# Optimization experiments

Measured on AMD Instinct MI355X. Metric: run time of the kernel, lower is better.

Reference implementation:

```python
import jax, jax.numpy as jnp
import numpy as np

K = 3       # kernel_size
STRIDE = 1
PAD = 1
EPS = 1e-12  # F.normalize eps


def setup_inputs() -> dict:
    key = jax.random.key(0)
    k1, k2, k3 = jax.random.split(key, 3)
    x = jax.random.normal(k1, (8, 128, 112, 112), dtype=jnp.float32)
    weight = jax.random.normal(k2, (256, 128, K, K), dtype=jnp.float32)
    bias = jax.random.normal(k3, (256,), dtype=jnp.float32)
    return {"x": x, "weight": weight, "bias": bias}


def reference(x, weight, bias):
    B, C, H, W = x.shape
    Cout = weight.shape[0]
    oh = (H + 2 * PAD - K) // STRIDE + 1
    ow = (W + 2 * PAD - K) // STRIDE + 1
    # im2col: [B, C*K*K, oh, ow]; feature order (C, kh, kw), same as torch F.unfold
    patches = jax.lax.conv_general_dilated_patches(
        x, (K, K), (STRIDE, STRIDE), [(PAD, PAD), (PAD, PAD)],
        dimension_numbers=("NCHW", "OIHW", "NCHW"))
    u = patches.reshape(B, C * K * K, oh * ow)
    # L2-normalize each patch column (dim=1), matching F.normalize(p=2, dim=1)
    norm = jnp.sqrt(jnp.sum(u * u, axis=1, keepdims=True))
    u = u / jnp.maximum(norm, EPS)
    # GEMM: [Cout, C*K*K] x [B, C*K*K, L] -> [B, Cout, L]
    out = jnp.einsum("od,bdl->bol", weight.reshape(Cout, -1), u)
    out = out.reshape(B, Cout, oh, ow) + bias[None, :, None, None]
    return out
```

## Files before the change

### kernel.cpp

```cpp
#include <hip/hip_runtime.h>

#define CIN    128
#define COUT   256
#define Hh     112
#define Ww     112
#define HW     12544
#define NBATCH 8
#define NPIX   (NBATCH*HW)
#define KD     (CIN*9)
#define PH     114
#define PPIX   (NBATCH*PH*PH)

typedef __bf16         v8bf __attribute__((ext_vector_type(8)));
typedef float          v4f  __attribute__((ext_vector_type(4)));

__device__ __forceinline__ unsigned short f2bf(float f) {
  unsigned int u = __float_as_uint(f);
  u += 0x7FFFu + ((u >> 16) & 1u);
  return (unsigned short)(u >> 16);
}

__device__ __forceinline__ void gl_lds16(const void* g, void* l) {
  __builtin_amdgcn_global_load_lds(
      (const __attribute__((address_space(1))) void*)g,
      (__attribute__((address_space(3))) void*)l, 16, 0, 0);
}

#define USS 130
__global__ __launch_bounds__(256) void k_pre(
    const float* __restrict__ x, const float* __restrict__ w,
    unsigned short* __restrict__ xbp, unsigned short* __restrict__ wpk,
    float* __restrict__ sq)
{
  __shared__ unsigned short US[112 * USS];
  __shared__ float sqp[112 * 4];

  int tid = threadIdx.x;
  int bid = blockIdx.x;

  if (bid >= NBATCH * PH) {
    int t = (bid - NBATCH * PH) * 2048 + tid * 8;
#pragma unroll
    for (int i = 0; i < 8; ++i) {
      int idx = t + i;
      int o  = idx / KD;
      int rr = idx - o * KD;
      int kk = rr >> 7;
      int c  = rr & 127;
      wpk[idx] = f2bf(w[(size_t)o * KD + c * 9 + kk]);
    }
    return;
  }

  int b  = bid / PH;
  int py = bid - b * PH;
  unsigned int* dstrow = (unsigned int*)xbp +
      (size_t)(b * PH + py) * PH * (CIN / 2);

  if (py == 0 || py == PH - 1) {
    uint4 z = {0, 0, 0, 0};
    for (int h = tid; h < PH * (CIN / 8); h += 256)
      *(uint4*)(dstrow + h * 4) = z;
    return;
  }

  int oy  = py - 1;
  int l   = tid & 63;
  int wid = tid >> 6;
  const float* xp = x + (size_t)b * CIN * HW + (size_t)oy * Ww;
  bool valid = l < 56;

  float a0 = 0.0f, a1 = 0.0f;
#pragma unroll
  for (int it = 0; it < 32; ++it) {
    int c = wid * 32 + it;
    float vx = 0.0f, vy = 0.0f;
    if (valid) {
      float2 v = *(const float2*)(xp + (size_t)c * HW + 2 * l);
      vx = v.x; vy = v.y;
    }
    a0 += vx * vx;
    a1 += vy * vy;
    if (valid) {
      US[(2 * l) * USS + c]     = f2bf(vx);
      US[(2 * l + 1) * USS + c] = f2bf(vy);
    }
  }
  if (valid) { sqp[(2 * l) * 4 + wid] = a0; sqp[(2 * l + 1) * 4 + wid] = a1; }
  __syncthreads();

  if (tid < 112) {
    float s = sqp[tid * 4] + sqp[tid * 4 + 1] + sqp[tid * 4 + 2] + sqp[tid * 4 + 3];
    sq[(size_t)b * HW + (size_t)oy * Ww + tid] = s;
  }

  unsigned int* dst = dstrow + (CIN / 2);
  for (int h = tid; h < 112 * 16; h += 256) {
    int px = h >> 4, part = h & 15;
    const unsigned short* s = &US[px * USS + part * 8];
    uint4 vv;
    vv.x = *(const unsigned int*)(s + 0);
    vv.y = *(const unsigned int*)(s + 2);
    vv.z = *(const unsigned int*)(s + 4);
    vv.w = *(const unsigned int*)(s + 6);
    *(uint4*)(dst + h * 4) = vv;
  }

  if (tid < 32) {
    uint4 z = {0, 0, 0, 0};
    int px   = (tid >> 4) ? (PH - 1) : 0;
    int part = tid & 15;
    *(uint4*)(dstrow + px * (CIN / 2) + part * 4) = z;
  }
}

#define SLAB_S 132
__global__ __launch_bounds__(256, 3) void k_conv(
    const unsigned short* __restrict__ wp,
    const unsigned short* __restrict__ xbp,
    const float* __restrict__ sq,
    const float* __restrict__ bias,
    float* __restrict__ out)
{
  __shared__ __align__(16) char smem[64 * SLAB_S * 4];
  unsigned short* As = (unsigned short*)smem;
  unsigned short* Bs = As + 128 * 64;
  float* slab = (float*)smem;

  int tid  = threadIdx.x;
  int lane = tid & 63;
  int wid  = tid >> 6;
  int wm   = wid >> 1, wn = wid & 1;
  int quad = lane >> 4;
  int l16  = lane & 15;

  int L  = blockIdx.x;
  int g  = L >> 4;
  int j  = L & 15;
  int bn = g * 8 + (j & 7);
  int bm = j >> 3;

  int srow = tid >> 3;
  int g16  = (tid & 7) ^ (srow & 7);

  const unsigned short* asrc = wp + (size_t)(bm * 128 + srow) * KD + g16 * 8;

  int pb[4];
#pragma unroll
  for (int jj = 0; jj < 4; ++jj) {
    int n  = bn * 128 + jj * 32 + srow;
    int b  = n / HW;  int r  = n - b * HW;
    int oy = r / Ww;  int ox = r - oy * Ww;
    pb[jj] = ((b * PH + oy) * PH + ox) * CIN + g16 * 8;
  }

  v4f acc[4][4];
#pragma unroll
  for (int mt = 0; mt < 4; ++mt)
#pragma unroll
    for (int nt = 0; nt < 4; ++nt)
#pragma unroll
      for (int q = 0; q < 4; ++q) acc[mt][nt][q] = 0.0f;

  const int khs[9] = {0,0,0,1,1,1,2,2,2};
  const int kws[9] = {0,1,2,0,1,2,0,1,2};

  for (int s = 0; s < 18; ++s) {
    int kk   = s >> 1;
    int c0   = (s & 1) * 64;
    int soff = (khs[kk] * PH + kws[kk]) * CIN + c0;

#pragma unroll
    for (int jj = 0; jj < 4; ++jj)
      gl_lds16(asrc + (size_t)jj * 32 * KD + s * 64,
               &As[(wid * 8 + jj * 32) * 64]);
#pragma unroll
    for (int jj = 0; jj < 4; ++jj)
      gl_lds16(xbp + pb[jj] + soff,
               &Bs[(wid * 8 + jj * 32) * 64]);

    __syncthreads();

#pragma unroll
    for (int h = 0; h < 2; ++h) {
      v8bf af[4], bf[4];
      int cch = (h * 4 + quad) ^ (l16 & 7);
#pragma unroll
      for (int mt = 0; mt < 4; ++mt)
        af[mt] = *(const v8bf*)&As[(wm * 64 + mt * 16 + l16) * 64 + cch * 8];
#pragma unroll
      for (int nt = 0; nt < 4; ++nt)
        bf[nt] = *(const v8bf*)&Bs[(wn * 64 + nt * 16 + l16) * 64 + cch * 8];
#pragma unroll
      for (int mt = 0; mt < 4; ++mt)
#pragma unroll
        for (int nt = 0; nt < 4; ++nt)
          acc[mt][nt] = __builtin_amdgcn_mfma_f32_16x16x32_bf16(
              af[mt], bf[nt], acc[mt][nt], 0, 0, 0);
    }

    __syncthreads();
  }

  int nbase = bn * 128;

  float invv[4];
#pragma unroll
  for (int nt = 0; nt < 4; ++nt) {
    int n  = nbase + wn * 64 + nt * 16 + l16;
    int b  = n / HW;  int r  = n - b * HW;
    int oy = r / Ww;  int ox = r - oy * Ww;
    const float* s = sq + (size_t)b * HW;
    float a2 = 0.0f;
#pragma unroll
    for (int dy = -1; dy <= 1; ++dy) {
      int iy = oy + dy;
      if (iy < 0 || iy >= Hh) continue;
#pragma unroll
      for (int dx = -1; dx <= 1; ++dx) {
        int ix = ox + dx;
        if (ix < 0 || ix >= Ww) continue;
        a2 += s[iy * Ww + ix];
      }
    }
    invv[nt] = 1.0f / fmaxf(sqrtf(a2), 1e-12f);
  }

  int bb = nbase / HW;
  int rr = nbase - bb * HW;
  float* obase = out + (size_t)bb * COUT * HW + rr;

  for (int pass = 0; pass < 2; ++pass) {
    if (pass) __syncthreads();
    if (wm == pass) {
#pragma unroll
      for (int mt = 0; mt < 4; ++mt)
#pragma unroll
        for (int nt = 0; nt < 4; ++nt) {
          int col = wn * 64 + nt * 16 + l16;
#pragma unroll
          for (int reg = 0; reg < 4; ++reg)
            slab[(mt * 16 + quad * 4 + reg) * SLAB_S + col] =
                acc[mt][nt][reg] * invv[nt];
        }
    }
    __syncthreads();
#pragma unroll
    for (int it = 0; it < 2; ++it) {
      int row = it * 32 + (tid >> 3);
      int o   = bm * 128 + pass * 64 + row;
      float bv = bias[o];
      float* orow = obase + (size_t)o * HW;
#pragma unroll
      for (int k = 0; k < 4; ++k) {
        int c4 = ((tid & 7) + k * 8) * 4;
        v4f v = *(const v4f*)&slab[row * SLAB_S + c4];
        v4f r2;
#pragma unroll
        for (int q = 0; q < 4; ++q) r2[q] = v[q] + bv;
        *(v4f*)(orow + c4) = r2;
      }
    }
  }
}

extern "C" void kernel_launch(void* const* d_in, const int* in_sizes, int n_in,
                              void* d_out, int out_size, void* d_ws, size_t ws_size,
                              hipStream_t stream) {
  const float* x    = (const float*)d_in[0];
  const float* w    = (const float*)d_in[1];
  const float* bias = (const float*)d_in[2];
  float* out        = (float*)d_out;

  char* ws = (char*)d_ws;
  unsigned short* xbp = (unsigned short*)ws;
  size_t off = (size_t)PPIX * CIN * 2;
  unsigned short* wpk = (unsigned short*)(ws + off);
  off += (size_t)COUT * KD * 2;
  float* sq = (float*)(ws + off);

  k_pre<<<NBATCH * PH + (COUT * KD) / 2048, 256, 0, stream>>>(x, w, xbp, wpk, sq);
  k_conv<<<1568, 256, 0, stream>>>(wpk, xbp, sq, bias, out);
}
```

Baseline: 217.2 us.

## Enlarge conv tile to 256x256 with double-buffered async LDS pipeline

The conv kernel moves from 128x128 tiles with 256 threads to 256x256 tiles with 512 threads, covering all output channels in one block (392 blocks). The K loop becomes double-buffered: it issues global-to-LDS loads for stage t+2 while computing stage t, using explicit vmcnt waits and raw barriers instead of full syncthreads, and raises MFMA priority with setprio. This is meant to hide load latency and double operand reuse per LDS byte, at the cost of 128KB of dynamic LDS, fewer blocks (under 1.3 waves on 256 CUs), and higher register pressure from 32 accumulators per thread.

```diff
diff --git a/kernel.cpp b/kernel.cpp
--- a/kernel.cpp
+++ b/kernel.cpp
@@ -114,95 +114,134 @@
   }
 }
 
-#define SLAB_S 132
-__global__ __launch_bounds__(256, 3) void k_conv(
+__device__ __forceinline__ void conv_tile(
+    unsigned short* Ab, unsigned short* Bb,
+    int t, bool do_stage,
+    v4f (&acc)[8][4], const int (&pb)[4],
+    const unsigned short* __restrict__ asrc,
+    const unsigned short* __restrict__ xbp,
+    int wm, int wn, int quad, int l16, int wid)
+{
+#pragma unroll
+  for (int h = 0; h < 2; ++h) {
+    v8bf bfr[4];
+    int cch = (h * 4 + quad) ^ (l16 & 7);
+#pragma unroll
+    for (int nt = 0; nt < 4; ++nt)
+      bfr[nt] = *(const v8bf*)&Bb[(wn * 64 + nt * 16 + l16) * 64 + cch * 8];
+#pragma unroll
+    for (int mh = 0; mh < 2; ++mh) {
+      v8bf af[4];
+#pragma unroll
+      for (int m2 = 0; m2 < 4; ++m2)
+        af[m2] = *(const v8bf*)&Ab[(wm * 128 + (mh * 4 + m2) * 16 + l16) * 64 + cch * 8];
+      __builtin_amdgcn_s_setprio(1);
+#pragma unroll
+      for (int m2 = 0; m2 < 4; ++m2)
+#pragma unroll
+        for (int nt = 0; nt < 4; ++nt)
+          acc[mh * 4 + m2][nt] = __builtin_amdgcn_mfma_f32_16x16x32_bf16(
+              af[m2], bfr[nt], acc[mh * 4 + m2][nt], 0, 0, 0);
+      __builtin_amdgcn_s_setprio(0);
+    }
+  }
+  __builtin_amdgcn_sched_barrier(0);
+  __builtin_amdgcn_s_barrier();
+  __builtin_amdgcn_sched_barrier(0);
+  if (do_stage) {
+    int t2 = t + 2;
+    int kk = t2 >> 1;
+    int kh = kk / 3, kw = kk - 3 * kh;
+    int soff = (kh * PH + kw) * CIN + (t2 & 1) * 64;
+#pragma unroll
+    for (int jj = 0; jj < 4; ++jj)
+      gl_lds16(asrc + (size_t)jj * 64 * KD + t2 * 64,
+               &Ab[(jj * 64 + wid * 8) * 64]);
+#pragma unroll
+    for (int jj = 0; jj < 4; ++jj)
+      gl_lds16(xbp + pb[jj] + soff,
+               &Bb[(jj * 64 + wid * 8) * 64]);
+    asm volatile("s_waitcnt vmcnt(8)" ::: "memory");
+  } else {
+    asm volatile("s_waitcnt vmcnt(0)" ::: "memory");
+  }
+  __builtin_amdgcn_sched_barrier(0);
+  __builtin_amdgcn_s_barrier();
+  __builtin_amdgcn_sched_barrier(0);
+}
+
+#define SLAB2 260
+__global__ __launch_bounds__(512, 2) void k_conv(
     const unsigned short* __restrict__ wp,
     const unsigned short* __restrict__ xbp,
     const float* __restrict__ sq,
     const float* __restrict__ bias,
     float* __restrict__ out)
 {
-  __shared__ __align__(16) char smem[64 * SLAB_S * 4];
-  unsigned short* As = (unsigned short*)smem;
-  unsigned short* Bs = As + 128 * 64;
+  extern __shared__ __align__(16) char smem[];
+  unsigned short* As0 = (unsigned short*)smem;
+  unsigned short* Bs0 = As0 + 256 * 64;
+  unsigned short* As1 = Bs0 + 256 * 64;
+  unsigned short* Bs1 = As1 + 256 * 64;
   float* slab = (float*)smem;
 
   int tid  = threadIdx.x;
   int lane = tid & 63;
   int wid  = tid >> 6;
-  int wm   = wid >> 1, wn = wid & 1;
+  int wm   = wid >> 2;
+  int wn   = wid & 3;
   int quad = lane >> 4;
   int l16  = lane & 15;
 
   int L  = blockIdx.x;
-  int g  = L >> 4;
-  int j  = L & 15;
-  int bn = g * 8 + (j & 7);
-  int bm = j >> 3;
+  int bn = (L & 7) * 49 + (L >> 3);
+  int nbase = bn * 256;
 
   int srow = tid >> 3;
   int g16  = (tid & 7) ^ (srow & 7);
 
-  const unsigned short* asrc = wp + (size_t)(bm * 128 + srow) * KD + g16 * 8;
+  const unsigned short* asrc = wp + (size_t)srow * KD + g16 * 8;
 
   int pb[4];
 #pragma unroll
   for (int jj = 0; jj < 4; ++jj) {
-    int n  = bn * 128 + jj * 32 + srow;
+    int n  = nbase + jj * 64 + srow;
     int b  = n / HW;  int r  = n - b * HW;
     int oy = r / Ww;  int ox = r - oy * Ww;
     pb[jj] = ((b * PH + oy) * PH + ox) * CIN + g16 * 8;
   }
 
-  v4f acc[4][4];
-#pragma unroll
-  for (int mt = 0; mt < 4; ++mt)
+  v4f acc[8][4];
+#pragma unroll
+  for (int mt = 0; mt < 8; ++mt)
 #pragma unroll
     for (int nt = 0; nt < 4; ++nt)
 #pragma unroll
       for (int q = 0; q < 4; ++q) acc[mt][nt][q] = 0.0f;
 
-  const int khs[9] = {0,0,0,1,1,1,2,2,2};
-  const int kws[9] = {0,1,2,0,1,2,0,1,2};
-
-  for (int s = 0; s < 18; ++s) {
-    int kk   = s >> 1;
-    int c0   = (s & 1) * 64;
-    int soff = (khs[kk] * PH + kws[kk]) * CIN + c0;
-
-#pragma unroll
-    for (int jj = 0; jj < 4; ++jj)
-      gl_lds16(asrc + (size_t)jj * 32 * KD + s * 64,
-               &As[(wid * 8 + jj * 32) * 64]);
-#pragma unroll
-    for (int jj = 0; jj < 4; ++jj)
-      gl_lds16(xbp + pb[jj] + soff,
-               &Bs[(wid * 8 + jj * 32) * 64]);
-
-    __syncthreads();
-
-#pragma unroll
-    for (int h = 0; h < 2; ++h) {
-      v8bf af[4], bf[4];
-      int cch = (h * 4 + quad) ^ (l16 & 7);
-#pragma unroll
-      for (int mt = 0; mt < 4; ++mt)
-        af[mt] = *(const v8bf*)&As[(wm * 64 + mt * 16 + l16) * 64 + cch * 8];
-#pragma unroll
-      for (int nt = 0; nt < 4; ++nt)
-        bf[nt] = *(const v8bf*)&Bs[(wn * 64 + nt * 16 + l16) * 64 + cch * 8];
-#pragma unroll
-      for (int mt = 0; mt < 4; ++mt)
-#pragma unroll
-        for (int nt = 0; nt < 4; ++nt)
-          acc[mt][nt] = __builtin_amdgcn_mfma_f32_16x16x32_bf16(
-              af[mt], bf[nt], acc[mt][nt], 0, 0, 0);
-    }
-
-    __syncthreads();
-  }
-
-  int nbase = bn * 128;
+#pragma unroll
+  for (int jj = 0; jj < 4; ++jj)
+    gl_lds16(asrc + (size_t)jj * 64 * KD, &As0[(jj * 64 + wid * 8) * 64]);
+#pragma unroll
+  for (int jj = 0; jj < 4; ++jj)
+    gl_lds16(xbp + pb[jj], &Bs0[(jj * 64 + wid * 8) * 64]);
+#pragma unroll
+  for (int jj = 0; jj < 4; ++jj)
+    gl_lds16(asrc + (size_t)jj * 64 * KD + 64, &As1[(jj * 64 + wid * 8) * 64]);
+#pragma unroll
+  for (int jj = 0; jj < 4; ++jj)
+    gl_lds16(xbp + pb[jj] + 64, &Bs1[(jj * 64 + wid * 8) * 64]);
+  asm volatile("s_waitcnt vmcnt(8)" ::: "memory");
+  __builtin_amdgcn_sched_barrier(0);
+  __builtin_amdgcn_s_barrier();
+  __builtin_amdgcn_sched_barrier(0);
+
+  for (int i = 0; i < 8; ++i) {
+    conv_tile(As0, Bs0, 2 * i,     true, acc, pb, asrc, xbp, wm, wn, quad, l16, wid);
+    conv_tile(As1, Bs1, 2 * i + 1, true, acc, pb, asrc, xbp, wm, wn, quad, l16, wid);
+  }
+  conv_tile(As0, Bs0, 16, false, acc, pb, asrc, xbp, wm, wn, quad, l16, wid);
+  conv_tile(As1, Bs1, 17, false, acc, pb, asrc, xbp, wm, wn, quad, l16, wid);
 
   float invv[4];
 #pragma unroll
@@ -230,36 +269,35 @@
   int rr = nbase - bb * HW;
   float* obase = out + (size_t)bb * COUT * HW + rr;
 
-  for (int pass = 0; pass < 2; ++pass) {
-    if (pass) __syncthreads();
-    if (wm == pass) {
-#pragma unroll
-      for (int mt = 0; mt < 4; ++mt)
+#pragma unroll
+  for (int p = 0; p < 4; ++p) {
+    if (p) __syncthreads();
+    if (wm == (p >> 1)) {
+      int base_mt = (p & 1) * 4;
+#pragma unroll
+      for (int m2 = 0; m2 < 4; ++m2)
 #pragma unroll
         for (int nt = 0; nt < 4; ++nt) {
           int col = wn * 64 + nt * 16 + l16;
 #pragma unroll
           for (int reg = 0; reg < 4; ++reg)
-            slab[(mt * 16 + quad * 4 + reg) * SLAB_S + col] =
-                acc[mt][nt][reg] * invv[nt];
+            slab[(m2 * 16 + quad * 4 + reg) * SLAB2 + col] =
+                acc[base_mt + m2][nt][reg] * invv[nt];
         }
     }
     __syncthreads();
-#pragma unroll
-    for (int it = 0; it < 2; ++it) {
-      int row = it * 32 + (tid >> 3);
-      int o   = bm * 128 + pass * 64 + row;
-      float bv = bias[o];
-      float* orow = obase + (size_t)o * HW;
-#pragma unroll
-      for (int k = 0; k < 4; ++k) {
-        int c4 = ((tid & 7) + k * 8) * 4;
-        v4f v = *(const v4f*)&slab[row * SLAB_S + c4];
-        v4f r2;
-#pragma unroll
-        for (int q = 0; q < 4; ++q) r2[q] = v[q] + bv;
-        *(v4f*)(orow + c4) = r2;
-      }
+    int r  = tid >> 3;
+    int o  = p * 64 + r;
+    float bv = bias[o];
+    float* orow = obase + (size_t)o * HW;
+#pragma unroll
+    for (int k = 0; k < 8; ++k) {
+      int c4 = (tid & 7) * 4 + k * 32;
+      v4f v = *(const v4f*)&slab[r * SLAB2 + c4];
+      v4f r2;
+#pragma unroll
+      for (int q = 0; q < 4; ++q) r2[q] = v[q] + bv;
+      *(v4f*)(orow + c4) = r2;
     }
   }
 }
@@ -279,6 +317,13 @@
   off += (size_t)COUT * KD * 2;
   float* sq = (float*)(ws + off);
 
+  static bool attr_done = false;
+  if (!attr_done) {
+    hipFuncSetAttribute((const void*)k_conv,
+                        hipFuncAttributeMaxDynamicSharedMemorySize, 131072);
+    attr_done = true;
+  }
+
   k_pre<<<NBATCH * PH + (COUT * KD) / 2048, 256, 0, stream>>>(x, w, xbp, wpk, sq);
-  k_conv<<<1568, 256, 0, stream>>>(wpk, xbp, sq, bias, out);
-}
+  k_conv<<<392, 512, 131072, stream>>>(wpk, xbp, sq, bias, out);
+}
```

After: 219.2 us. No clear change (+0.9%).

## Stage a shared input-row window in LDS and reuse it across kernel-width taps

Applied to the files above, without the earlier changes.

The conv kernel used to fetch a fresh 128-pixel by 64-channel B tile from global memory for each of the 18 (tap, channel-half) steps. It now loads one swizzled window of 144 padded pixel slots by all 128 channels per kernel row. Each per-lane B fragment is read at a per-pixel slot offset plus the kw shift, so the window serves all three horizontal taps. This cuts global and L2 traffic for activations roughly threefold. In exchange, LDS use grows to about 52 KB per block, which is tight for three blocks per CU, and the swizzled window reads may cause extra bank conflicts.

```diff
diff --git a/kernel.cpp b/kernel.cpp
--- a/kernel.cpp
+++ b/kernel.cpp
@@ -10,6 +10,7 @@
 #define KD     (CIN*9)
 #define PH     114
 #define PPIX   (NBATCH*PH*PH)
+#define WSLOT  144
 
 typedef __bf16         v8bf __attribute__((ext_vector_type(8)));
 typedef float          v4f  __attribute__((ext_vector_type(4)));
@@ -122,9 +123,9 @@
     const float* __restrict__ bias,
     float* __restrict__ out)
 {
-  __shared__ __align__(16) char smem[64 * SLAB_S * 4];
-  unsigned short* As = (unsigned short*)smem;
-  unsigned short* Bs = As + 128 * 64;
+  __shared__ __align__(16) char smem[WSLOT * CIN * 2 + 128 * 64 * 2];
+  unsigned short* win = (unsigned short*)smem;
+  unsigned short* As  = win + WSLOT * CIN;
   float* slab = (float*)smem;
 
   int tid  = threadIdx.x;
@@ -142,16 +143,21 @@
 
   int srow = tid >> 3;
   int g16  = (tid & 7) ^ (srow & 7);
-
   const unsigned short* asrc = wp + (size_t)(bm * 128 + srow) * KD + g16 * 8;
 
-  int pb[4];
-#pragma unroll
-  for (int jj = 0; jj < 4; ++jj) {
-    int n  = bn * 128 + jj * 32 + srow;
-    int b  = n / HW;  int r  = n - b * HW;
-    int oy = r / Ww;  int ox = r - oy * Ww;
-    pb[jj] = ((b * PH + oy) * PH + ox) * CIN + g16 * 8;
+  int nbase = bn * 128;
+  int b  = nbase / HW;
+  int r  = nbase - b * HW;
+  int oy0 = r / Ww;  int ox0 = r - oy0 * Ww;
+  int slot0 = (oy0 + 1) * PH + ox0 + 1;
+  const unsigned short* xbpB = xbp + (size_t)b * PH * PH * CIN;
+
+  int soff[4];
+#pragma unroll
+  for (int nt = 0; nt < 4; ++nt) {
+    int rl = r + wn * 64 + nt * 16 + l16;
+    int oy = rl / Ww;  int ox = rl - oy * Ww;
+    soff[nt] = (oy + 1) * PH + ox + 1 - slot0;
   }
 
   v4f acc[4][4];
@@ -162,55 +168,62 @@
 #pragma unroll
       for (int q = 0; q < 4; ++q) acc[mt][nt][q] = 0.0f;
 
-  const int khs[9] = {0,0,0,1,1,1,2,2,2};
-  const int kws[9] = {0,1,2,0,1,2,0,1,2};
-
-  for (int s = 0; s < 18; ++s) {
-    int kk   = s >> 1;
-    int c0   = (s & 1) * 64;
-    int soff = (khs[kk] * PH + kws[kk]) * CIN + c0;
-
-#pragma unroll
-    for (int jj = 0; jj < 4; ++jj)
-      gl_lds16(asrc + (size_t)jj * 32 * KD + s * 64,
-               &As[(wid * 8 + jj * 32) * 64]);
-#pragma unroll
-    for (int jj = 0; jj < 4; ++jj)
-      gl_lds16(xbp + pb[jj] + soff,
-               &Bs[(wid * 8 + jj * 32) * 64]);
-
-    __syncthreads();
-
-#pragma unroll
-    for (int h = 0; h < 2; ++h) {
-      v8bf af[4], bf[4];
-      int cch = (h * 4 + quad) ^ (l16 & 7);
-#pragma unroll
-      for (int mt = 0; mt < 4; ++mt)
-        af[mt] = *(const v8bf*)&As[(wm * 64 + mt * 16 + l16) * 64 + cch * 8];
-#pragma unroll
-      for (int nt = 0; nt < 4; ++nt)
-        bf[nt] = *(const v8bf*)&Bs[(wn * 64 + nt * 16 + l16) * 64 + cch * 8];
-#pragma unroll
-      for (int mt = 0; mt < 4; ++mt)
-#pragma unroll
-        for (int nt = 0; nt < 4; ++nt)
-          acc[mt][nt] = __builtin_amdgcn_mfma_f32_16x16x32_bf16(
-              af[mt], bf[nt], acc[mt][nt], 0, 0, 0);
-    }
-
-    __syncthreads();
-  }
-
-  int nbase = bn * 128;
+  for (int kh = 0; kh < 3; ++kh) {
+    int S0 = slot0 + (kh - 1) * PH - 1;
+    const unsigned short* bsrc = xbpB + (size_t)S0 * CIN;
+#pragma unroll
+    for (int i = 0; i < 9; ++i) {
+      int ch = (i * 4 + wid) * 64 + lane;
+      int sl = ch >> 4, p = ch & 15;
+      gl_lds16(bsrc + (size_t)sl * CIN + (p ^ (sl & 7)) * 8,
+               &win[(i * 4 + wid) * 512]);
+    }
+
+#pragma unroll
+    for (int h2 = 0; h2 < 2; ++h2) {
+#pragma unroll
+      for (int kw = 0; kw < 3; ++kw) {
+        int aoff = (kh * 3 + kw) * 128 + h2 * 64;
+#pragma unroll
+        for (int jj = 0; jj < 4; ++jj)
+          gl_lds16(asrc + (size_t)jj * 32 * KD + aoff,
+                   &As[(wid * 8 + jj * 32) * 64]);
+
+        __syncthreads();
+
+#pragma unroll
+        for (int h = 0; h < 2; ++h) {
+          v8bf af[4], bfr[4];
+          int cchA = (h * 4 + quad) ^ (l16 & 7);
+#pragma unroll
+          for (int mt = 0; mt < 4; ++mt)
+            af[mt] = *(const v8bf*)&As[(wm * 64 + mt * 16 + l16) * 64 + cchA * 8];
+          int cb = h2 * 8 + h * 4 + quad;
+#pragma unroll
+          for (int nt = 0; nt < 4; ++nt) {
+            int sl = soff[nt] + kw;
+            bfr[nt] = *(const v8bf*)&win[sl * CIN + (cb ^ (sl & 7)) * 8];
+          }
+#pragma unroll
+          for (int mt = 0; mt < 4; ++mt)
+#pragma unroll
+            for (int nt = 0; nt < 4; ++nt)
+              acc[mt][nt] = __builtin_amdgcn_mfma_f32_16x16x32_bf16(
+                  af[mt], bfr[nt], acc[mt][nt], 0, 0, 0);
+        }
+
+        __syncthreads();
+      }
+    }
+  }
 
   float invv[4];
 #pragma unroll
   for (int nt = 0; nt < 4; ++nt) {
     int n  = nbase + wn * 64 + nt * 16 + l16;
-    int b  = n / HW;  int r  = n - b * HW;
-    int oy = r / Ww;  int ox = r - oy * Ww;
-    const float* s = sq + (size_t)b * HW;
+    int bb2 = n / HW;  int rr2 = n - bb2 * HW;
+    int oy = rr2 / Ww;  int ox = rr2 - oy * Ww;
+    const float* s = sq + (size_t)bb2 * HW;
     float a2 = 0.0f;
 #pragma unroll
     for (int dy = -1; dy <= 1; ++dy) {
```

New measurement: 245.3 us. 1.13x slower.
